# Kernel optimization log

Measured on AMD Instinct MI355X. Metric: run time of the kernel, lower is better.

## Reference

```python
import jax, jax.numpy as jnp
import numpy as np

WEIGHT_THRESH = 0.5
EPS = 1e-5
B, N = 4096, 1024


def setup_inputs() -> dict:
    key = jax.random.key(0)
    k1, k2, k3 = jax.random.split(key, 3)
    src = jax.random.normal(k1, (B, N, 3), dtype=jnp.float32)
    tgt = jax.random.normal(k2, (B, N, 3), dtype=jnp.float32)
    w = jax.random.uniform(k3, (B, N), dtype=jnp.float32)
    return {"src_points": src, "tgt_points": tgt, "weights": w}


def _weighted_procrustes(src, ref, w):
    # threshold + normalize weights
    w = jnp.where(w < WEIGHT_THRESH, jnp.zeros_like(w), w)
    w = w / (jnp.sum(w, axis=1, keepdims=True) + EPS)
    w = w[:, :, None]                       # (B, N, 1)
    # weighted centroids
    src_c = jnp.sum(src * w, axis=1, keepdims=True)   # (B, 1, 3)
    ref_c = jnp.sum(ref * w, axis=1, keepdims=True)   # (B, 1, 3)
    src0 = src - src_c
    ref0 = ref - ref_c
    # weighted cross-covariance H = src0^T @ (w * ref0): (B, 3, 3)
    H = jnp.einsum('bni,bnj->bij', src0, w * ref0)
    U, S, Vh = jnp.linalg.svd(H)            # torch.svd returns V, jnp returns Vh
    V = jnp.swapaxes(Vh, 1, 2)
    Ut = jnp.swapaxes(U, 1, 2)
    det = jnp.linalg.det(V @ Ut)            # (B,)
    sgn = jnp.sign(det)
    # D = diag(1, 1, sign(det)); V @ D scales the last column of V
    D = jnp.stack([jnp.ones_like(sgn), jnp.ones_like(sgn), sgn], axis=-1)  # (B, 3)
    R = (V * D[:, None, :]) @ Ut            # (B, 3, 3)
    # t = ref_c - R @ src_c
    t = (jnp.swapaxes(ref_c, 1, 2) - R @ jnp.swapaxes(src_c, 1, 2))[:, :, 0]  # (B, 3)
    return R, t


def reference(src_points, tgt_points, weights):
    return _weighted_procrustes(src_points, tgt_points, weights)
```

## Files before the change

### kernel.cpp

```cpp
#include <hip/hip_runtime.h>
#include <math.h>

#define WTHRESH 0.5f
#define EPSV    1e-5f

#define JROT(app,aqq,apq, arp,arq, vAp,vAq, vBp,vBq, vCp,vCq)                 \
  do {                                                                        \
    float _apq = (apq);                                                       \
    if (fabsf(_apq) > 1e-30f) {                                               \
      float _tau = ((aqq) - (app)) * 0.5f / _apq;                             \
      float _t = copysignf(1.0f, _tau) / (fabsf(_tau) + sqrtf(1.0f + _tau*_tau)); \
      float _c = 1.0f / sqrtf(1.0f + _t*_t);                                  \
      float _s = _t * _c;                                                     \
      float _app = (app), _aqq = (aqq);                                       \
      (app) = _app - _t * _apq;                                               \
      (aqq) = _aqq + _t * _apq;                                               \
      (apq) = 0.0f;                                                           \
      float _arp = (arp), _arq = (arq);                                       \
      (arp) = _c * _arp - _s * _arq;                                          \
      (arq) = _s * _arp + _c * _arq;                                          \
      { float _vp=(vAp), _vq=(vAq); (vAp)=_c*_vp-_s*_vq; (vAq)=_s*_vp+_c*_vq; } \
      { float _vp=(vBp), _vq=(vBq); (vBp)=_c*_vp-_s*_vq; (vBq)=_s*_vp+_c*_vq; } \
      { float _vp=(vCp), _vq=(vCq); (vCp)=_c*_vp-_s*_vq; (vCq)=_s*_vp+_c*_vq; } \
    }                                                                         \
  } while (0)

#define CSWAP(li,lj, x0,x1, y0,y1, z0,z1)                                     \
  do { if ((li) < (lj)) {                                                     \
    float _t;                                                                 \
    _t=(li); (li)=(lj); (lj)=_t;                                              \
    _t=(x0); (x0)=(x1); (x1)=_t;                                              \
    _t=(y0); (y0)=(y1); (y1)=_t;                                              \
    _t=(z0); (z0)=(z1); (z1)=_t;                                              \
  } } while (0)

__global__ __launch_bounds__(256) void wproc_kernel(
    const float* __restrict__ src, const float* __restrict__ tgt,
    const float* __restrict__ wts, float* __restrict__ outR,
    float* __restrict__ outT)
{
  const int b   = blockIdx.x;
  const int tid = threadIdx.x;

  const float4* s4 = reinterpret_cast<const float4*>(src + (size_t)b * 3072);
  const float4* t4 = reinterpret_cast<const float4*>(tgt + (size_t)b * 3072);
  const float4* w4 = reinterpret_cast<const float4*>(wts + (size_t)b * 1024);

  float4 sA = s4[3*tid+0], sB = s4[3*tid+1], sC = s4[3*tid+2];
  float4 tA = t4[3*tid+0], tB = t4[3*tid+1], tC = t4[3*tid+2];
  float4 wv = w4[tid];

  float acc[16];
  #pragma unroll
  for (int k = 0; k < 16; ++k) acc[k] = 0.0f;

  float PX[4][3] = {{sA.x,sA.y,sA.z},{sA.w,sB.x,sB.y},{sB.z,sB.w,sC.x},{sC.y,sC.z,sC.w}};
  float PY[4][3] = {{tA.x,tA.y,tA.z},{tA.w,tB.x,tB.y},{tB.z,tB.w,tC.x},{tC.y,tC.z,tC.w}};
  float WW[4]    = {wv.x, wv.y, wv.z, wv.w};

  #pragma unroll
  for (int k = 0; k < 4; ++k) {
    float w  = (WW[k] < WTHRESH) ? 0.0f : WW[k];
    float x0 = PX[k][0], x1 = PX[k][1], x2 = PX[k][2];
    float y0 = PY[k][0], y1 = PY[k][1], y2 = PY[k][2];
    acc[0] += w;
    acc[1] += w*x0; acc[2] += w*x1; acc[3] += w*x2;
    acc[4] += w*y0; acc[5] += w*y1; acc[6] += w*y2;
    float wx0 = w*x0, wx1 = w*x1, wx2 = w*x2;
    acc[7]  += wx0*y0; acc[8]  += wx0*y1; acc[9]  += wx0*y2;
    acc[10] += wx1*y0; acc[11] += wx1*y1; acc[12] += wx1*y2;
    acc[13] += wx2*y0; acc[14] += wx2*y1; acc[15] += wx2*y2;
  }

  #pragma unroll
  for (int off = 32; off > 0; off >>= 1) {
    #pragma unroll
    for (int k = 0; k < 16; ++k) acc[k] += __shfl_down(acc[k], off, 64);
  }

  __shared__ float red[4][16];
  const int wave = tid >> 6;
  const int lane = tid & 63;
  if (lane == 0) {
    #pragma unroll
    for (int k = 0; k < 16; ++k) red[wave][k] = acc[k];
  }
  __syncthreads();
  if (tid != 0) return;

  float f[16];
  #pragma unroll
  for (int k = 0; k < 16; ++k) f[k] = red[0][k] + red[1][k] + red[2][k] + red[3][k];

  const float inv  = 1.0f / (f[0] + EPSV);
  const float cx0 = f[1]*inv, cx1 = f[2]*inv, cx2 = f[3]*inv;
  const float cy0 = f[4]*inv, cy1 = f[5]*inv, cy2 = f[6]*inv;
  const float ssum = f[0] * inv;
  const float g = 2.0f - ssum;

  float H00 = f[7]*inv  - g*cx0*cy0, H01 = f[8]*inv  - g*cx0*cy1, H02 = f[9]*inv  - g*cx0*cy2;
  float H10 = f[10]*inv - g*cx1*cy0, H11 = f[11]*inv - g*cx1*cy1, H12 = f[12]*inv - g*cx1*cy2;
  float H20 = f[13]*inv - g*cx2*cy0, H21 = f[14]*inv - g*cx2*cy1, H22 = f[15]*inv - g*cx2*cy2;

  float a00 = H00*H00 + H10*H10 + H20*H20;
  float a11 = H01*H01 + H11*H11 + H21*H21;
  float a22 = H02*H02 + H12*H12 + H22*H22;
  float a01 = H00*H01 + H10*H11 + H20*H21;
  float a02 = H00*H02 + H10*H12 + H20*H22;
  float a12 = H01*H02 + H11*H12 + H21*H22;

  float v00=1.f,v01=0.f,v02=0.f, v10=0.f,v11=1.f,v12=0.f, v20=0.f,v21=0.f,v22=1.f;

  #pragma unroll
  for (int sweep = 0; sweep < 8; ++sweep) {
    JROT(a00,a11,a01, a02,a12, v00,v01, v10,v11, v20,v21);
    JROT(a00,a22,a02, a01,a12, v00,v02, v10,v12, v20,v22);
    JROT(a11,a22,a12, a01,a02, v01,v02, v11,v12, v21,v22);
  }

  CSWAP(a00,a11, v00,v01, v10,v11, v20,v21);
  CSWAP(a00,a22, v00,v02, v10,v12, v20,v22);
  CSWAP(a11,a22, v01,v02, v11,v12, v21,v22);

  float u00 = H00*v00 + H01*v10 + H02*v20;
  float u10 = H10*v00 + H11*v10 + H12*v20;
  float u20 = H20*v00 + H21*v10 + H22*v20;
  float u01 = H00*v01 + H01*v11 + H02*v21;
  float u11 = H10*v01 + H11*v11 + H12*v21;
  float u21 = H20*v01 + H21*v11 + H22*v21;
  float u02 = H00*v02 + H01*v12 + H02*v22;
  float u12 = H10*v02 + H11*v12 + H12*v22;
  float u22 = H20*v02 + H21*v12 + H22*v22;

  float n0 = sqrtf(u00*u00 + u10*u10 + u20*u20);
  float n1 = sqrtf(u01*u01 + u11*u11 + u21*u21);
  float n2 = sqrtf(u02*u02 + u12*u12 + u22*u22);

  float R00,R01,R02,R10,R11,R12,R20,R21,R22;

  if (n0 < 1e-20f) {
    R00=1.f;R01=0.f;R02=0.f; R10=0.f;R11=1.f;R12=0.f; R20=0.f;R21=0.f;R22=1.f;
  } else {
    float i0 = 1.0f / n0;
    u00*=i0; u10*=i0; u20*=i0;

    if (n1 > 1e-7f * n0) {
      float i1 = 1.0f / n1;
      u01*=i1; u11*=i1; u21*=i1;
    } else {
      float ax = fabsf(u00), ay = fabsf(u10), az = fabsf(u20);
      float e0,e1,e2;
      if (ax <= ay && ax <= az)      { e0=1.f; e1=0.f; e2=0.f; }
      else if (ay <= az)             { e0=0.f; e1=1.f; e2=0.f; }
      else                           { e0=0.f; e1=0.f; e2=1.f; }
      u01 = u10*e2 - u20*e1;
      u11 = u20*e0 - u00*e2;
      u21 = u00*e1 - u10*e0;
      float nn = 1.0f / sqrtf(u01*u01 + u11*u11 + u21*u21);
      u01*=nn; u11*=nn; u21*=nn;
    }

    if (n2 > 1e-7f * n0) {
      float i2 = 1.0f / n2;
      u02*=i2; u12*=i2; u22*=i2;
    } else {
      u02 = u10*u21 - u20*u11;
      u12 = u20*u01 - u00*u21;
      u22 = u00*u11 - u10*u01;
    }

    float detU = u00*(u11*u22 - u12*u21) - u01*(u10*u22 - u12*u20) + u02*(u10*u21 - u11*u20);
    float detV = v00*(v11*v22 - v12*v21) - v01*(v10*v22 - v12*v20) + v02*(v10*v21 - v11*v20);
    float sgn = (detU * detV < 0.0f) ? -1.0f : 1.0f;

    R00 = v00*u00 + v01*u01 + sgn*v02*u02;
    R01 = v00*u10 + v01*u11 + sgn*v02*u12;
    R02 = v00*u20 + v01*u21 + sgn*v02*u22;
    R10 = v10*u00 + v11*u01 + sgn*v12*u02;
    R11 = v10*u10 + v11*u11 + sgn*v12*u12;
    R12 = v10*u20 + v11*u21 + sgn*v12*u22;
    R20 = v20*u00 + v21*u01 + sgn*v22*u02;
    R21 = v20*u10 + v21*u11 + sgn*v22*u12;
    R22 = v20*u20 + v21*u21 + sgn*v22*u22;
  }

  float t0 = cy0 - (R00*cx0 + R01*cx1 + R02*cx2);
  float t1 = cy1 - (R10*cx0 + R11*cx1 + R12*cx2);
  float t2 = cy2 - (R20*cx0 + R21*cx1 + R22*cx2);

  float* Rb = outR + (size_t)b * 9;
  Rb[0]=R00; Rb[1]=R01; Rb[2]=R02;
  Rb[3]=R10; Rb[4]=R11; Rb[5]=R12;
  Rb[6]=R20; Rb[7]=R21; Rb[8]=R22;
  float* tb = outT + (size_t)b * 3;
  tb[0]=t0; tb[1]=t1; tb[2]=t2;
}

extern "C" void kernel_launch(void* const* d_in, const int* in_sizes, int n_in,
                              void* d_out, int out_size, void* d_ws, size_t ws_size,
                              hipStream_t stream) {
  const float* src = (const float*)d_in[0];
  const float* tgt = (const float*)d_in[1];
  const float* w   = (const float*)d_in[2];

  const int B = in_sizes[2] / 1024;
  float* outR = (float*)d_out;
  float* outT = outR + (size_t)B * 9;

  wproc_kernel<<<dim3(B), dim3(256), 0, stream>>>(src, tgt, w, outR, outT);
}
```

Measured before the change: 145.4 us.

## Split reduction and SVD into two kernels and use DPP wave reductions

Measured after the change: 140.7 us. -3.3%, faster.

```diff
diff --git a/kernel.cpp b/kernel.cpp
--- a/kernel.cpp
+++ b/kernel.cpp
@@ -3,6 +3,13 @@
 
 #define WTHRESH 0.5f
 #define EPSV    1e-5f
+
+template <int CTRL>
+__device__ __forceinline__ float dpp_add(float x) {
+  int xi = __builtin_bit_cast(int, x);
+  int mv = __builtin_amdgcn_update_dpp(0, xi, CTRL, 0xF, 0xF, true);
+  return x + __builtin_bit_cast(float, mv);
+}
 
 #define JROT(app,aqq,apq, arp,arq, vAp,vAq, vBp,vBq, vCp,vCq)                 \
   do {                                                                        \
@@ -34,10 +41,9 @@
     _t=(z0); (z0)=(z1); (z1)=_t;                                              \
   } } while (0)
 
-__global__ __launch_bounds__(256) void wproc_kernel(
+__global__ __launch_bounds__(256) void wproc_reduce(
     const float* __restrict__ src, const float* __restrict__ tgt,
-    const float* __restrict__ wts, float* __restrict__ outR,
-    float* __restrict__ outT)
+    const float* __restrict__ wts, float* __restrict__ ws)
 {
   const int b   = blockIdx.x;
   const int tid = threadIdx.x;
@@ -73,24 +79,36 @@
   }
 
   #pragma unroll
-  for (int off = 32; off > 0; off >>= 1) {
+  for (int k = 0; k < 16; ++k) acc[k] = dpp_add<0x111>(acc[k]);
+  #pragma unroll
+  for (int k = 0; k < 16; ++k) acc[k] = dpp_add<0x112>(acc[k]);
+  #pragma unroll
+  for (int k = 0; k < 16; ++k) acc[k] = dpp_add<0x114>(acc[k]);
+  #pragma unroll
+  for (int k = 0; k < 16; ++k) acc[k] = dpp_add<0x118>(acc[k]);
+  #pragma unroll
+  for (int k = 0; k < 16; ++k) acc[k] = dpp_add<0x142>(acc[k]);
+  #pragma unroll
+  for (int k = 0; k < 16; ++k) acc[k] = dpp_add<0x143>(acc[k]);
+
+  if ((tid & 63) == 63) {
+    float* o = ws + ((size_t)b * 4 + (tid >> 6)) * 16;
     #pragma unroll
-    for (int k = 0; k < 16; ++k) acc[k] += __shfl_down(acc[k], off, 64);
-  }
-
-  __shared__ float red[4][16];
-  const int wave = tid >> 6;
-  const int lane = tid & 63;
-  if (lane == 0) {
-    #pragma unroll
-    for (int k = 0; k < 16; ++k) red[wave][k] = acc[k];
-  }
-  __syncthreads();
-  if (tid != 0) return;
-
+    for (int k = 0; k < 16; ++k) o[k] = acc[k];
+  }
+}
+
+__global__ __launch_bounds__(256) void wproc_svd(
+    const float* __restrict__ ws, float* __restrict__ outR,
+    float* __restrict__ outT, int B)
+{
+  const int b = blockIdx.x * 256 + threadIdx.x;
+  if (b >= B) return;
+
+  const float* p = ws + (size_t)b * 64;
   float f[16];
   #pragma unroll
-  for (int k = 0; k < 16; ++k) f[k] = red[0][k] + red[1][k] + red[2][k] + red[3][k];
+  for (int k = 0; k < 16; ++k) f[k] = p[k] + p[16 + k] + p[32 + k] + p[48 + k];
 
   const float inv  = 1.0f / (f[0] + EPSV);
   const float cx0 = f[1]*inv, cx1 = f[2]*inv, cx2 = f[3]*inv;
@@ -206,6 +224,8 @@
   const int B = in_sizes[2] / 1024;
   float* outR = (float*)d_out;
   float* outT = outR + (size_t)B * 9;
-
-  wproc_kernel<<<dim3(B), dim3(256), 0, stream>>>(src, tgt, w, outR, outT);
-}
+  float* ws   = (float*)d_ws;
+
+  wproc_reduce<<<dim3(B), dim3(256), 0, stream>>>(src, tgt, w, ws);
+  wproc_svd<<<dim3((B + 255) / 256), dim3(256), 0, stream>>>(ws, outR, outT, B);
+}
```
